# Performance work log

Measured on AMD Instinct MI355X. Metric: run time of the kernel, lower is better.

The kernel has to match this reference:

```python
import jax, jax.numpy as jnp
import numpy as np

B, PD, CD = 8192, 1024, 1024


def setup_inputs() -> dict:
    key = jax.random.key(0)
    ks = jax.random.split(key, 10)
    u = lambda k, shape: jax.random.uniform(k, shape, dtype=jnp.float32, minval=-0.05, maxval=0.05)
    return {
        "P": jax.random.normal(ks[0], (B, PD), dtype=jnp.float32),
        "C1": jax.random.normal(ks[1], (B, CD), dtype=jnp.float32),
        "C2": jax.random.normal(ks[2], (B, CD), dtype=jnp.float32),
        "C3": jax.random.normal(ks[3], (B, CD), dtype=jnp.float32),
        "C4": jax.random.normal(ks[4], (B, CD), dtype=jnp.float32),
        "GateWeight_P": u(ks[5], (PD, CD)),
        "GateWeight_C": u(ks[6], (CD, CD)),
        "GateBias": u(ks[7], (CD,)),
        "OutWeight": u(ks[8], (PD, CD)),
        "OutBias": u(ks[9], (CD, 1)),
    }


def reference(P, C1, C2, C3, C4, GateWeight_P, GateWeight_C, GateBias, OutWeight, OutBias):
    # Stack the 4 choice branches: [4, B, C]
    Cs = jnp.stack([C1, C2, C3, C4], axis=0)
    WP = P @ GateWeight_P                                  # [B, C]
    WC = jnp.einsum("kbc,cd->kbd", Cs, GateWeight_C)       # [4, B, C]
    g = jax.nn.sigmoid(WP[None] + WC + GateBias)           # [4, B, C]
    C_dash = Cs * g                                        # [4, B, C]
    WP_out = P @ OutWeight                                 # [B, C]
    scores = jnp.einsum("kbc,bc->kb", C_dash, WP_out)      # batch_dot axes=[1,1]
    bias = jnp.einsum("kbc,c->kb", C_dash, OutBias[:, 0])  # K.dot(C_dash, OutBias)
    return (scores + bias).T                               # [B, 4]
```

## Files before the change

kernel.cpp:

```cpp
#include <hip/hip_runtime.h>
#include <hip/hip_bf16.h>


#define B_  8192
#define PD_ 1024
#define CD_ 1024

typedef unsigned short ushort_t;
typedef __attribute__((ext_vector_type(8))) short    short8;
typedef __attribute__((ext_vector_type(8))) unsigned short ushort8;
typedef __attribute__((ext_vector_type(4))) float    floatx4;

__device__ __forceinline__ float bf2f(unsigned short u) {
    return __uint_as_float(((unsigned)u) << 16);
}
__device__ __forceinline__ unsigned short f2bf(float f) {
    unsigned u = __float_as_uint(f);
    unsigned r = u + 0x7FFFu + ((u >> 16) & 1u);
    return (unsigned short)(r >> 16);
}

__global__ __launch_bounds__(256) void prep_kernel(const float* __restrict__ P,
                                                   const float* __restrict__ C1,
                                                   const float* __restrict__ C2,
                                                   const float* __restrict__ C3,
                                                   const float* __restrict__ C4,
                                                   const float* __restrict__ GWP,
                                                   const float* __restrict__ OW,
                                                   const float* __restrict__ GWC,
                                                   ushort_t* __restrict__ Pb,
                                                   ushort_t* __restrict__ Call,
                                                   ushort_t* __restrict__ Wcat,
                                                   ushort_t* __restrict__ GWCt,
                                                   float* __restrict__ out) {
    const int bid = blockIdx.x;
    const int tid = threadIdx.x;
    if (bid < 40960) {
        const int seg = bid >> 13;
        const int i   = (bid & 8191) * 256 + tid;
        const float* src;
        ushort_t* dst;
        switch (seg) {
            case 0: src = P;  dst = Pb; break;
            case 1: src = C1; dst = Call; break;
            case 2: src = C2; dst = Call + (size_t)1 * B_ * CD_; break;
            case 3: src = C3; dst = Call + (size_t)2 * B_ * CD_; break;
            default: src = C4; dst = Call + (size_t)3 * B_ * CD_; break;
        }
        float4 v = ((const float4*)src)[i];
        ushort4 o;
        o.x = f2bf(v.x); o.y = f2bf(v.y); o.z = f2bf(v.z); o.w = f2bf(v.w);
        ((ushort4*)dst)[i] = o;
    } else if (bid < 44032) {
        __shared__ float tile[32][33];
        const int tb  = bid - 40960;
        const int seg = tb >> 10;
        const int t32 = tb & 1023;
        const float* src;
        ushort_t* dst;
        switch (seg) {
            case 0: src = GWP; dst = Wcat; break;
            case 1: src = OW;  dst = Wcat + 1024 * 1024; break;
            default: src = GWC; dst = GWCt; break;
        }
        const int c0 = (t32 & 31) * 32, r0 = (t32 >> 5) * 32;
        const int x = tid & 31, y = tid >> 5;
        for (int i = y; i < 32; i += 8)
            tile[i][x] = src[(size_t)(r0 + i) * 1024 + c0 + x];
        __syncthreads();
        for (int i = y; i < 32; i += 8)
            dst[(size_t)(c0 + i) * 1024 + r0 + x] = f2bf(tile[x][i]);
    } else {
        const int i = (bid - 44032) * 256 + tid;
        ((float4*)out)[i] = float4{0.f, 0.f, 0.f, 0.f};
    }
}

__device__ __forceinline__ void gl_lds16(const void* g, void* l) {
    __builtin_amdgcn_global_load_lds((const __attribute__((address_space(1))) void*)g,
                                     (__attribute__((address_space(3))) void*)l, 16, 0, 0);
}

__global__ __launch_bounds__(256) void gemmA(const ushort_t* __restrict__ A,
                                             const ushort_t* __restrict__ Bt,
                                             ushort_t* __restrict__ C) {
    __shared__ ushort_t lA[128 * 32];
    __shared__ ushort_t lB[128 * 32];
    const int K = 1024, N = 2048;
    const int tileN = (blockIdx.x & 15) * 128, tileM = (blockIdx.x >> 4) * 128;

    const int t = threadIdx.x;
    const int wave = t >> 6, lane = t & 63;
    const int quad = lane >> 4, l16 = lane & 15;
    const int wm = wave >> 1, wn = wave & 1;

    const int ch0  = wave * 2;
    const int srow = lane >> 2;
    const int sc   = ((lane & 3) ^ ((lane >> 4) & 3)) * 8;
    const int lo0  = ch0 * 512 + lane * 8;

    const ushort_t* Ag0 = A  + (size_t)(tileM + ch0 * 16 + srow)      * K + sc;
    const ushort_t* Ag1 = A  + (size_t)(tileM + ch0 * 16 + srow + 16) * K + sc;
    const ushort_t* Bg0 = Bt + (size_t)(tileN + ch0 * 16 + srow)      * K + sc;
    const ushort_t* Bg1 = Bt + (size_t)(tileN + ch0 * 16 + srow + 16) * K + sc;

    const int fro = (l16 * 4 + (quad ^ (l16 >> 2))) * 8;

    floatx4 acc[4][4];
#pragma unroll
    for (int i = 0; i < 4; i++)
#pragma unroll
        for (int j = 0; j < 4; j++) acc[i][j] = (floatx4)0.f;

    for (int k0 = 0; k0 < K; k0 += 32) {
        gl_lds16(Ag0 + k0, &lA[lo0]);
        gl_lds16(Ag1 + k0, &lA[lo0 + 512]);
        gl_lds16(Bg0 + k0, &lB[lo0]);
        gl_lds16(Bg1 + k0, &lB[lo0 + 512]);
        __syncthreads();
        short8 af[4], bfr[4];
#pragma unroll
        for (int mi = 0; mi < 4; mi++)
            af[mi] = *(const short8*)&lA[(wm * 4 + mi) * 512 + fro];
#pragma unroll
        for (int ni = 0; ni < 4; ni++)
            bfr[ni] = *(const short8*)&lB[(wn * 4 + ni) * 512 + fro];
#pragma unroll
        for (int mi = 0; mi < 4; mi++)
#pragma unroll
            for (int ni = 0; ni < 4; ni++)
                acc[mi][ni] = __builtin_amdgcn_mfma_f32_16x16x32_bf16(
                    af[mi], bfr[ni], acc[mi][ni], 0, 0, 0);
        __syncthreads();
    }
#pragma unroll
    for (int mi = 0; mi < 4; mi++)
#pragma unroll
        for (int ni = 0; ni < 4; ni++)
#pragma unroll
            for (int r = 0; r < 4; r++) {
                int row = tileM + wm * 64 + mi * 16 + quad * 4 + r;
                int col = tileN + wn * 64 + ni * 16 + l16;
                C[(size_t)row * N + col] = f2bf(acc[mi][ni][r]);
            }
}

__global__ __launch_bounds__(256) void gemmB_fused(const ushort_t* __restrict__ Call,
                                                   const ushort_t* __restrict__ GWCt,
                                                   const ushort_t* __restrict__ WPcat,
                                                   const float* __restrict__ Gb,
                                                   const float* __restrict__ Ob,
                                                   float* __restrict__ out) {
    __shared__ ushort_t smem[128 * 136];
    ushort_t* lA = smem;
    ushort_t* lB = smem + 4096;
    const int K = 1024;
    const int tileN = (blockIdx.x & 7) * 128, tileM = (blockIdx.x >> 3) * 128;

    const int t = threadIdx.x;
    const int wave = t >> 6, lane = t & 63;
    const int quad = lane >> 4, l16 = lane & 15;
    const int wm = wave >> 1, wn = wave & 1;

    const int ch0  = wave * 2;
    const int srow = lane >> 2;
    const int sc   = ((lane & 3) ^ ((lane >> 4) & 3)) * 8;
    const int lo0  = ch0 * 512 + lane * 8;

    const ushort_t* Ag0 = Call + (size_t)(tileM + ch0 * 16 + srow)      * K + sc;
    const ushort_t* Ag1 = Call + (size_t)(tileM + ch0 * 16 + srow + 16) * K + sc;
    const ushort_t* Bg0 = GWCt + (size_t)(tileN + ch0 * 16 + srow)      * K + sc;
    const ushort_t* Bg1 = GWCt + (size_t)(tileN + ch0 * 16 + srow + 16) * K + sc;

    const int fro = (l16 * 4 + (quad ^ (l16 >> 2))) * 8;

    floatx4 acc[4][4];
#pragma unroll
    for (int i = 0; i < 4; i++)
#pragma unroll
        for (int j = 0; j < 4; j++) acc[i][j] = (floatx4)0.f;

    for (int k0 = 0; k0 < K; k0 += 32) {
        gl_lds16(Ag0 + k0, &lA[lo0]);
        gl_lds16(Ag1 + k0, &lA[lo0 + 512]);
        gl_lds16(Bg0 + k0, &lB[lo0]);
        gl_lds16(Bg1 + k0, &lB[lo0 + 512]);
        __syncthreads();
        short8 af[4], bfr[4];
#pragma unroll
        for (int mi = 0; mi < 4; mi++)
            af[mi] = *(const short8*)&lA[(wm * 4 + mi) * 512 + fro];
#pragma unroll
        for (int ni = 0; ni < 4; ni++)
            bfr[ni] = *(const short8*)&lB[(wn * 4 + ni) * 512 + fro];
#pragma unroll
        for (int mi = 0; mi < 4; mi++)
#pragma unroll
            for (int ni = 0; ni < 4; ni++)
                acc[mi][ni] = __builtin_amdgcn_mfma_f32_16x16x32_bf16(
                    af[mi], bfr[ni], acc[mi][ni], 0, 0, 0);
        __syncthreads();
    }

#pragma unroll
    for (int mi = 0; mi < 4; mi++)
#pragma unroll
        for (int ni = 0; ni < 4; ni++)
#pragma unroll
            for (int r = 0; r < 4; r++) {
                int rl = wm * 64 + mi * 16 + quad * 4 + r;
                int cl = wn * 64 + ni * 16 + l16;
                smem[rl * 136 + cl] = f2bf(acc[mi][ni][r]);
            }
    __syncthreads();

    const int rl   = t >> 1;
    const int grow = tileM + rl;
    const int kbr  = grow >> 13;
    const int b    = grow & 8191;
    const int ch   = (t & 1) * 64;

    float s = 0.f;
#pragma unroll
    for (int j = 0; j < 8; j++) {
        const int cl   = ch + j * 8;
        const int gcol = tileN + cl;
        ushort8 wc8  = *(const ushort8*)&smem[rl * 136 + cl];
        ushort8 wp8  = *(const ushort8*)&WPcat[(size_t)b * 2048 + gcol];
        ushort8 wpo8 = *(const ushort8*)&WPcat[(size_t)b * 2048 + 1024 + gcol];
        ushort8 ck8  = *(const ushort8*)&Call[(size_t)grow * 1024 + gcol];
        floatx4 g0 = *(const floatx4*)&Gb[gcol];
        floatx4 g1 = *(const floatx4*)&Gb[gcol + 4];
        floatx4 o0 = *(const floatx4*)&Ob[gcol];
        floatx4 o1 = *(const floatx4*)&Ob[gcol + 4];
        float gb[8], ob[8];
#pragma unroll
        for (int q = 0; q < 4; q++) { gb[q] = g0[q]; gb[4 + q] = g1[q]; ob[q] = o0[q]; ob[4 + q] = o1[q]; }
#pragma unroll
        for (int q = 0; q < 8; q++) {
            float x = bf2f(wp8[q]) + bf2f(wc8[q]) + gb[q];
            float g = 1.f / (1.f + __expf(-x));
            s += bf2f(ck8[q]) * g * (bf2f(wpo8[q]) + ob[q]);
        }
    }
    s += __shfl_xor(s, 1);
    if ((t & 1) == 0)
        atomicAdd(&out[(size_t)b * 4 + kbr], s);
}

extern "C" void kernel_launch(void* const* d_in, const int* in_sizes, int n_in,
                              void* d_out, int out_size, void* d_ws, size_t ws_size,
                              hipStream_t stream) {
    (void)in_sizes; (void)n_in; (void)out_size; (void)ws_size;
    const float* P   = (const float*)d_in[0];
    const float* C1  = (const float*)d_in[1];
    const float* C2  = (const float*)d_in[2];
    const float* C3  = (const float*)d_in[3];
    const float* C4  = (const float*)d_in[4];
    const float* GWP = (const float*)d_in[5];
    const float* GWC = (const float*)d_in[6];
    const float* Gb  = (const float*)d_in[7];
    const float* OW  = (const float*)d_in[8];
    const float* Ob  = (const float*)d_in[9];
    float* out = (float*)d_out;

    char* ws = (char*)d_ws;
    ushort_t* Pb    = (ushort_t*)(ws);
    ushort_t* Call  = (ushort_t*)(ws + (16u << 20));
    ushort_t* Wcat  = (ushort_t*)(ws + (80u << 20));
    ushort_t* GWCt  = (ushort_t*)(ws + (84u << 20));
    ushort_t* WPcat = (ushort_t*)(ws + (86u << 20));

    prep_kernel<<<44064, 256, 0, stream>>>(P, C1, C2, C3, C4, GWP, OW, GWC,
                                           Pb, Call, Wcat, GWCt, out);
    gemmA<<<1024, 256, 0, stream>>>(Pb, Wcat, WPcat);
    gemmB_fused<<<2048, 256, 0, stream>>>(Call, GWCt, WPcat, Gb, Ob, out);
}
```

Before: 420.8 us.

## Use 128x256 tiles with 8 waves and XCD-aware block mapping in both GEMMs

Both GEMM kernels move from 256-thread blocks with 128x128 tiles to 512-thread blocks with 128x256 tiles. The A tile is now shared across twice as many output columns, and block indices are remapped so each XCD works on contiguous row tiles. The fused epilogue in gemmB now stages the wider accumulator through shared memory in two halves, with four threads per row reducing via shuffles. The aim is to cut global and L2 traffic per FLOP. In exchange there are extra barriers in the epilogue, and the larger blocks may lower occupancy.

```diff
diff --git a/kernel.cpp b/kernel.cpp
--- a/kernel.cpp
+++ b/kernel.cpp
@@ -81,29 +81,29 @@
                                      (__attribute__((address_space(3))) void*)l, 16, 0, 0);
 }
 
-__global__ __launch_bounds__(256) void gemmA(const ushort_t* __restrict__ A,
-                                             const ushort_t* __restrict__ Bt,
-                                             ushort_t* __restrict__ C) {
-    __shared__ ushort_t lA[128 * 32];
-    __shared__ ushort_t lB[128 * 32];
+__global__ __launch_bounds__(512, 4) void gemmA(const ushort_t* __restrict__ A,
+                                                const ushort_t* __restrict__ Bt,
+                                                ushort_t* __restrict__ C) {
+    __shared__ ushort_t smem[12288];
+    ushort_t* lA = smem;
+    ushort_t* lB = smem + 4096;
     const int K = 1024, N = 2048;
-    const int tileN = (blockIdx.x & 15) * 128, tileM = (blockIdx.x >> 4) * 128;
+    const int xcd = blockIdx.x & 7, q = blockIdx.x >> 3;
+    const int tileM = ((q >> 3) * 8 + xcd) * 128;
+    const int tileN = (q & 7) * 256;
 
     const int t = threadIdx.x;
     const int wave = t >> 6, lane = t & 63;
     const int quad = lane >> 4, l16 = lane & 15;
-    const int wm = wave >> 1, wn = wave & 1;
-
-    const int ch0  = wave * 2;
+    const int wm = wave >> 2, wn = wave & 3;
+
     const int srow = lane >> 2;
     const int sc   = ((lane & 3) ^ ((lane >> 4) & 3)) * 8;
-    const int lo0  = ch0 * 512 + lane * 8;
-
-    const ushort_t* Ag0 = A  + (size_t)(tileM + ch0 * 16 + srow)      * K + sc;
-    const ushort_t* Ag1 = A  + (size_t)(tileM + ch0 * 16 + srow + 16) * K + sc;
-    const ushort_t* Bg0 = Bt + (size_t)(tileN + ch0 * 16 + srow)      * K + sc;
-    const ushort_t* Bg1 = Bt + (size_t)(tileN + ch0 * 16 + srow + 16) * K + sc;
-
+    const ushort_t* Ag  = A  + (size_t)(tileM + wave * 16 + srow) * K + sc;
+    const ushort_t* Bg0 = Bt + (size_t)(tileN + wave * 32 + srow) * K + sc;
+    const ushort_t* Bg1 = Bg0 + (size_t)16 * K;
+    const int loA = wave * 512 + lane * 8;
+    const int loB = wave * 1024 + lane * 8;
     const int fro = (l16 * 4 + (quad ^ (l16 >> 2))) * 8;
 
     floatx4 acc[4][4];
@@ -113,10 +113,9 @@
         for (int j = 0; j < 4; j++) acc[i][j] = (floatx4)0.f;
 
     for (int k0 = 0; k0 < K; k0 += 32) {
-        gl_lds16(Ag0 + k0, &lA[lo0]);
-        gl_lds16(Ag1 + k0, &lA[lo0 + 512]);
-        gl_lds16(Bg0 + k0, &lB[lo0]);
-        gl_lds16(Bg1 + k0, &lB[lo0 + 512]);
+        gl_lds16(Ag + k0,  &lA[loA]);
+        gl_lds16(Bg0 + k0, &lB[loB]);
+        gl_lds16(Bg1 + k0, &lB[loB + 512]);
         __syncthreads();
         short8 af[4], bfr[4];
 #pragma unroll
@@ -145,33 +144,32 @@
             }
 }
 
-__global__ __launch_bounds__(256) void gemmB_fused(const ushort_t* __restrict__ Call,
-                                                   const ushort_t* __restrict__ GWCt,
-                                                   const ushort_t* __restrict__ WPcat,
-                                                   const float* __restrict__ Gb,
-                                                   const float* __restrict__ Ob,
-                                                   float* __restrict__ out) {
+__global__ __launch_bounds__(512, 4) void gemmB_fused(const ushort_t* __restrict__ Call,
+                                                      const ushort_t* __restrict__ GWCt,
+                                                      const ushort_t* __restrict__ WPcat,
+                                                      const float* __restrict__ Gb,
+                                                      const float* __restrict__ Ob,
+                                                      float* __restrict__ out) {
     __shared__ ushort_t smem[128 * 136];
     ushort_t* lA = smem;
     ushort_t* lB = smem + 4096;
     const int K = 1024;
-    const int tileN = (blockIdx.x & 7) * 128, tileM = (blockIdx.x >> 3) * 128;
+    const int xcd = blockIdx.x & 7, q = blockIdx.x >> 3;
+    const int tileM = ((q >> 2) * 8 + xcd) * 128;
+    const int tileN = (q & 3) * 256;
 
     const int t = threadIdx.x;
     const int wave = t >> 6, lane = t & 63;
     const int quad = lane >> 4, l16 = lane & 15;
-    const int wm = wave >> 1, wn = wave & 1;
-
-    const int ch0  = wave * 2;
+    const int wm = wave >> 2, wn = wave & 3;
+
     const int srow = lane >> 2;
     const int sc   = ((lane & 3) ^ ((lane >> 4) & 3)) * 8;
-    const int lo0  = ch0 * 512 + lane * 8;
-
-    const ushort_t* Ag0 = Call + (size_t)(tileM + ch0 * 16 + srow)      * K + sc;
-    const ushort_t* Ag1 = Call + (size_t)(tileM + ch0 * 16 + srow + 16) * K + sc;
-    const ushort_t* Bg0 = GWCt + (size_t)(tileN + ch0 * 16 + srow)      * K + sc;
-    const ushort_t* Bg1 = GWCt + (size_t)(tileN + ch0 * 16 + srow + 16) * K + sc;
-
+    const ushort_t* Ag  = Call + (size_t)(tileM + wave * 16 + srow) * K + sc;
+    const ushort_t* Bg0 = GWCt + (size_t)(tileN + wave * 32 + srow) * K + sc;
+    const ushort_t* Bg1 = Bg0 + (size_t)16 * K;
+    const int loA = wave * 512 + lane * 8;
+    const int loB = wave * 1024 + lane * 8;
     const int fro = (l16 * 4 + (quad ^ (l16 >> 2))) * 8;
 
     floatx4 acc[4][4];
@@ -181,10 +179,9 @@
         for (int j = 0; j < 4; j++) acc[i][j] = (floatx4)0.f;
 
     for (int k0 = 0; k0 < K; k0 += 32) {
-        gl_lds16(Ag0 + k0, &lA[lo0]);
-        gl_lds16(Ag1 + k0, &lA[lo0 + 512]);
-        gl_lds16(Bg0 + k0, &lB[lo0]);
-        gl_lds16(Bg1 + k0, &lB[lo0 + 512]);
+        gl_lds16(Ag + k0,  &lA[loA]);
+        gl_lds16(Bg0 + k0, &lB[loB]);
+        gl_lds16(Bg1 + k0, &lB[loB + 512]);
         __syncthreads();
         short8 af[4], bfr[4];
 #pragma unroll
@@ -202,49 +199,55 @@
         __syncthreads();
     }
 
-#pragma unroll
-    for (int mi = 0; mi < 4; mi++)
-#pragma unroll
-        for (int ni = 0; ni < 4; ni++)
-#pragma unroll
-            for (int r = 0; r < 4; r++) {
-                int rl = wm * 64 + mi * 16 + quad * 4 + r;
-                int cl = wn * 64 + ni * 16 + l16;
-                smem[rl * 136 + cl] = f2bf(acc[mi][ni][r]);
-            }
-    __syncthreads();
-
-    const int rl   = t >> 1;
+    const int rl   = t >> 2;
+    const int cq   = (t & 3) * 32;
     const int grow = tileM + rl;
     const int kbr  = grow >> 13;
     const int b    = grow & 8191;
-    const int ch   = (t & 1) * 64;
-
     float s = 0.f;
-#pragma unroll
-    for (int j = 0; j < 8; j++) {
-        const int cl   = ch + j * 8;
-        const int gcol = tileN + cl;
-        ushort8 wc8  = *(const ushort8*)&smem[rl * 136 + cl];
-        ushort8 wp8  = *(const ushort8*)&WPcat[(size_t)b * 2048 + gcol];
-        ushort8 wpo8 = *(const ushort8*)&WPcat[(size_t)b * 2048 + 1024 + gcol];
-        ushort8 ck8  = *(const ushort8*)&Call[(size_t)grow * 1024 + gcol];
-        floatx4 g0 = *(const floatx4*)&Gb[gcol];
-        floatx4 g1 = *(const floatx4*)&Gb[gcol + 4];
-        floatx4 o0 = *(const floatx4*)&Ob[gcol];
-        floatx4 o1 = *(const floatx4*)&Ob[gcol + 4];
-        float gb[8], ob[8];
-#pragma unroll
-        for (int q = 0; q < 4; q++) { gb[q] = g0[q]; gb[4 + q] = g1[q]; ob[q] = o0[q]; ob[4 + q] = o1[q]; }
-#pragma unroll
-        for (int q = 0; q < 8; q++) {
-            float x = bf2f(wp8[q]) + bf2f(wc8[q]) + gb[q];
-            float g = 1.f / (1.f + __expf(-x));
-            s += bf2f(ck8[q]) * g * (bf2f(wpo8[q]) + ob[q]);
+
+#pragma unroll
+    for (int h = 0; h < 2; h++) {
+        __syncthreads();
+        if ((wn >> 1) == h) {
+#pragma unroll
+            for (int mi = 0; mi < 4; mi++)
+#pragma unroll
+                for (int ni = 0; ni < 4; ni++)
+#pragma unroll
+                    for (int r = 0; r < 4; r++) {
+                        int rlw = wm * 64 + mi * 16 + quad * 4 + r;
+                        int clw = (wn & 1) * 64 + ni * 16 + l16;
+                        smem[rlw * 136 + clw] = f2bf(acc[mi][ni][r]);
+                    }
+        }
+        __syncthreads();
+#pragma unroll
+        for (int j = 0; j < 4; j++) {
+            const int cl   = cq + j * 8;
+            const int gcol = tileN + h * 128 + cl;
+            ushort8 wc8  = *(const ushort8*)&smem[rl * 136 + cl];
+            ushort8 wp8  = *(const ushort8*)&WPcat[(size_t)b * 2048 + gcol];
+            ushort8 wpo8 = *(const ushort8*)&WPcat[(size_t)b * 2048 + 1024 + gcol];
+            ushort8 ck8  = *(const ushort8*)&Call[(size_t)grow * 1024 + gcol];
+            floatx4 g0 = *(const floatx4*)&Gb[gcol];
+            floatx4 g1 = *(const floatx4*)&Gb[gcol + 4];
+            floatx4 o0 = *(const floatx4*)&Ob[gcol];
+            floatx4 o1 = *(const floatx4*)&Ob[gcol + 4];
+            float gb[8], ob[8];
+#pragma unroll
+            for (int p = 0; p < 4; p++) { gb[p] = g0[p]; gb[4 + p] = g1[p]; ob[p] = o0[p]; ob[4 + p] = o1[p]; }
+#pragma unroll
+            for (int p = 0; p < 8; p++) {
+                float x = bf2f(wp8[p]) + bf2f(wc8[p]) + gb[p];
+                float g = 1.f / (1.f + __expf(-x));
+                s += bf2f(ck8[p]) * g * (bf2f(wpo8[p]) + ob[p]);
+            }
         }
     }
     s += __shfl_xor(s, 1);
-    if ((t & 1) == 0)
+    s += __shfl_xor(s, 2);
+    if ((t & 3) == 0)
         atomicAdd(&out[(size_t)b * 4 + kbr], s);
 }
 
@@ -273,6 +276,6 @@
 
     prep_kernel<<<44064, 256, 0, stream>>>(P, C1, C2, C3, C4, GWP, OW, GWC,
                                            Pb, Call, Wcat, GWCt, out);
-    gemmA<<<1024, 256, 0, stream>>>(Pb, Wcat, WPcat);
-    gemmB_fused<<<2048, 256, 0, stream>>>(Call, GWCt, WPcat, Gb, Ob, out);
-}
+    gemmA<<<512, 512, 0, stream>>>(Pb, Wcat, WPcat);
+    gemmB_fused<<<1024, 512, 0, stream>>>(Call, GWCt, WPcat, Gb, Ob, out);
+}
```

After: 398.2 us. -5.4%, faster.
